# Kernel optimization log

Hardware: AMD Instinct MI355X
Metric: run time of the kernel (lower is better)

The kernel has to match this reference:

```python
import jax, jax.numpy as jnp
import numpy as np

B, S, D, H = 2, 2048, 1024, 16
Dh = D // H
LN_EPS = 1e-5


def setup_inputs() -> dict:
    key = jax.random.key(0)
    ks = jax.random.split(key, 14)
    s = 1.0 / np.sqrt(D)
    return {
        "q": jax.random.normal(ks[0], (B, S, D), jnp.float32),
        "k": jax.random.normal(ks[1], (B, S, D), jnp.float32),
        "v": jax.random.normal(ks[2], (B, S, D), jnp.float32),
        "attn_mask": jax.random.randint(ks[3], (B, S, S), 0, 2).astype(bool),
        "Wq": jax.random.normal(ks[4], (D, D), jnp.float32) * s,
        "bq": jnp.zeros((D,), jnp.float32),
        "Wk": jax.random.normal(ks[5], (D, D), jnp.float32) * s,
        "bk": jnp.zeros((D,), jnp.float32),
        "Wv": jax.random.normal(ks[6], (D, D), jnp.float32) * s,
        "bv": jnp.zeros((D,), jnp.float32),
        "Wo": jax.random.normal(ks[7], (D, D), jnp.float32) * s,
        "bo": jnp.zeros((D,), jnp.float32),
        "gamma": jnp.ones((D,), jnp.float32),
        "beta": jnp.zeros((D,), jnp.float32),
    }


def reference(q, k, v, attn_mask, Wq, bq, Wk, bk, Wv, bv, Wo, bo, gamma, beta):
    residual = q
    # projections (W stored as [in, out])
    qh = (q @ Wq + bq).reshape(B, S, H, Dh).transpose(0, 2, 1, 3)  # [B,H,S,Dh]
    kh = (k @ Wk + bk).reshape(B, S, H, Dh).transpose(0, 2, 1, 3)
    vh = (v @ Wv + bv).reshape(B, S, H, Dh).transpose(0, 2, 1, 3)
    scores = jnp.einsum("bhqd,bhkd->bhqk", qh, kh) / np.sqrt(Dh)
    scores = jnp.where(attn_mask[:, None, :, :], -1e9, scores)
    attn = jax.nn.softmax(scores, axis=-1)  # dropout is identity in eval
    context = jnp.einsum("bhqk,bhkd->bhqd", attn, vh)  # [B,H,S,Dh]
    # faithful to original bug: flat reshape WITHOUT transposing heads back
    context = context.reshape(B, S, D)
    out = context @ Wo + bo
    x = residual + out
    mu = jnp.mean(x, axis=-1, keepdims=True)
    var = jnp.var(x, axis=-1, keepdims=True)
    out = (x - mu) / jnp.sqrt(var + LN_EPS) * gamma + beta
    return out, attn
```

## Files before the change

### kernel.cpp

```cpp
#include <hip/hip_runtime.h>
#include <hip/hip_bf16.h>

typedef __attribute__((ext_vector_type(8))) short bf16x8;
typedef __attribute__((ext_vector_type(4))) float f32x4;

__device__ __forceinline__ short f2bf(float f) {
    union { float f; unsigned u; } v; v.f = f;
    unsigned r = (v.u + 0x7FFFu + ((v.u >> 16) & 1u)) >> 16;
    return (short)r;
}
__device__ __forceinline__ float bf2f(short s) {
    union { unsigned u; float f; } v; v.u = ((unsigned)(unsigned short)s) << 16;
    return v.f;
}
__device__ __forceinline__ void gll16(const void* g, void* l) {
    __builtin_amdgcn_global_load_lds(
        (const __attribute__((address_space(1))) unsigned int*)g,
        (__attribute__((address_space(3))) unsigned int*)l, 16, 0, 0);
}

__global__ __launch_bounds__(256) void k_prep(
    const float* __restrict__ qin, const float* __restrict__ kin, const float* __restrict__ vin,
    short* __restrict__ qbf, short* __restrict__ kbf, short* __restrict__ vbf,
    const float* __restrict__ Wq, const float* __restrict__ Wk,
    const float* __restrict__ Wv, const float* __restrict__ Wo,
    short* __restrict__ WqT, short* __restrict__ WkT,
    short* __restrict__ WvT, short* __restrict__ WoT,
    const int* __restrict__ mask, unsigned* __restrict__ mb)
{
    __shared__ int sm[8192];
    const int bid = blockIdx.x, tid = threadIdx.x;
    if (bid < 6144) {
        const float* in = bid < 2048 ? qin : (bid < 4096 ? kin : vin);
        short* out = bid < 2048 ? qbf : (bid < 4096 ? kbf : vbf);
        const long i = ((long)(bid & 2047) * 256 + tid) * 8;
        float4 f0 = *reinterpret_cast<const float4*>(&in[i]);
        float4 f1 = *reinterpret_cast<const float4*>(&in[i + 4]);
        bf16x8 v;
        v[0] = f2bf(f0.x); v[1] = f2bf(f0.y); v[2] = f2bf(f0.z); v[3] = f2bf(f0.w);
        v[4] = f2bf(f1.x); v[5] = f2bf(f1.y); v[6] = f2bf(f1.z); v[7] = f2bf(f1.w);
        *reinterpret_cast<bf16x8*>(&out[i]) = v;
    } else if (bid < 10240) {
        const int t2 = bid - 6144, which = t2 >> 10, local = t2 & 1023;
        const float* W = which == 0 ? Wq : (which == 1 ? Wk : (which == 2 ? Wv : Wo));
        short* WT = which == 0 ? WqT : (which == 1 ? WkT : (which == 2 ? WvT : WoT));
        float (*t)[33] = reinterpret_cast<float(*)[33]>(sm);
        const int rb = (local >> 5) * 32, cb = (local & 31) * 32;
        const int tr = tid >> 3, tc = (tid & 7) * 4;
        const float4 v = *reinterpret_cast<const float4*>(&W[(long)(rb + tr) * 1024 + cb + tc]);
        t[tr][tc + 0] = v.x; t[tr][tc + 1] = v.y; t[tr][tc + 2] = v.z; t[tr][tc + 3] = v.w;
        __syncthreads();
        short4 o;
        o.x = f2bf(t[tc + 0][tr]); o.y = f2bf(t[tc + 1][tr]);
        o.z = f2bf(t[tc + 2][tr]); o.w = f2bf(t[tc + 3][tr]);
        *reinterpret_cast<short4*>(&WT[(long)(cb + tr) * 1024 + rb + tc]) = o;
    } else {
        const long base = (long)(bid - 10240) * 8192;
#pragma unroll
        for (int i = 0; i < 8; ++i)
            *reinterpret_cast<int4*>(&sm[i * 1024 + tid * 4]) =
                *reinterpret_cast<const int4*>(&mask[base + i * 1024 + tid * 4]);
        __syncthreads();
        unsigned wv = 0;
#pragma unroll
        for (int j = 0; j < 32; ++j) wv |= (sm[tid * 32 + j] != 0 ? 1u : 0u) << j;
        mb[base / 32 + tid] = wv;
    }
}

__global__ __launch_bounds__(256) void k_gemm_qkv(
    const short* __restrict__ A0, const short* __restrict__ A1, const short* __restrict__ A2,
    const short* __restrict__ B0, const short* __restrict__ B1, const short* __restrict__ B2,
    const float* __restrict__ b0, const float* __restrict__ b1, const float* __restrict__ b2,
    short* __restrict__ o0, short* __restrict__ o1, short* __restrict__ o2)
{
    __shared__ short As[128 * 64];
    __shared__ short Bs[128 * 64];
    const int z = blockIdx.z;
    const short* A = z == 0 ? A0 : (z == 1 ? A1 : A2);
    const short* BT = z == 0 ? B0 : (z == 1 ? B1 : B2);
    const float* bias = z == 0 ? b0 : (z == 1 ? b1 : b2);
    short* outp = z == 0 ? o0 : (z == 1 ? o1 : o2);
    const float scale = z == 0 ? 0.125f : 1.0f;

    const int tid = threadIdx.x, w = tid >> 6, lane = tid & 63;
    const int lr = lane & 15, lg = lane >> 4;
    const int rowbase = blockIdx.y * 128, colbase = blockIdx.x * 128;
    const int wr = (w >> 1) * 64, wc = (w & 1) * 64;
    const int srow = lane >> 3, sc_ = (lane & 7) ^ srow;

    f32x4 acc[4][4] = {};

    for (int kb = 0; kb < 1024; kb += 64) {
#pragma unroll
        for (int ii = 0; ii < 4; ++ii) {
            const int rl = w * 32 + ii * 8 + srow;
            gll16(A + (long)(rowbase + rl) * 1024 + kb + sc_ * 8, &As[(w * 32 + ii * 8) * 64]);
            gll16(BT + (long)(colbase + rl) * 1024 + kb + sc_ * 8, &Bs[(w * 32 + ii * 8) * 64]);
        }
        __syncthreads();
#pragma unroll
        for (int ks = 0; ks < 2; ++ks) {
            bf16x8 a[4], bq[4];
#pragma unroll
            for (int m = 0; m < 4; ++m) {
                const int r = wr + m * 16 + lr;
                a[m] = *reinterpret_cast<const bf16x8*>(&As[r * 64 + (((ks * 4 + lg) ^ (r & 7)) << 3)]);
            }
#pragma unroll
            for (int n = 0; n < 4; ++n) {
                const int r = wc + n * 16 + lr;
                bq[n] = *reinterpret_cast<const bf16x8*>(&Bs[r * 64 + (((ks * 4 + lg) ^ (r & 7)) << 3)]);
            }
#pragma unroll
            for (int m = 0; m < 4; ++m)
#pragma unroll
                for (int n = 0; n < 4; ++n)
                    acc[m][n] = __builtin_amdgcn_mfma_f32_16x16x32_bf16(a[m], bq[n], acc[m][n], 0, 0, 0);
        }
        __syncthreads();
    }

#pragma unroll
    for (int m = 0; m < 4; ++m) {
#pragma unroll
        for (int n = 0; n < 4; ++n) {
            const int C = colbase + wc + n * 16 + lr;
            const float bv = bias[C];
#pragma unroll
            for (int rr = 0; rr < 4; ++rr) {
                const int R = rowbase + wr + m * 16 + lg * 4 + rr;
                const float val = (acc[m][n][rr] + bv) * scale;
                const int b = R >> 11, s = R & 2047, h = C >> 6, dh = C & 63;
                if (z != 2)
                    outp[(((long)(b * 16 + h) * 2048 + s) << 6) + dh] = f2bf(val);
                else
                    outp[(((long)(b * 16 + h) * 64 + dh) << 11) + s] = f2bf(val);
            }
        }
    }
}

__global__ __launch_bounds__(256) void k_gemm_o(
    const short* __restrict__ A, const short* __restrict__ BT,
    const float* __restrict__ bias, const float* __restrict__ resid,
    float* __restrict__ outp)
{
    __shared__ short As[128 * 64];
    __shared__ short Bs[128 * 64];
    const int tid = threadIdx.x, w = tid >> 6, lane = tid & 63;
    const int lr = lane & 15, lg = lane >> 4;
    const int rowbase = blockIdx.y * 128, colbase = blockIdx.x * 128;
    const int wr = (w >> 1) * 64, wc = (w & 1) * 64;
    const int srow = lane >> 3, sc_ = (lane & 7) ^ srow;

    f32x4 acc[4][4] = {};

    for (int kb = 0; kb < 1024; kb += 64) {
#pragma unroll
        for (int ii = 0; ii < 4; ++ii) {
            const int rl = w * 32 + ii * 8 + srow;
            gll16(A + (long)(rowbase + rl) * 1024 + kb + sc_ * 8, &As[(w * 32 + ii * 8) * 64]);
            gll16(BT + (long)(colbase + rl) * 1024 + kb + sc_ * 8, &Bs[(w * 32 + ii * 8) * 64]);
        }
        __syncthreads();
#pragma unroll
        for (int ks = 0; ks < 2; ++ks) {
            bf16x8 a[4], bq[4];
#pragma unroll
            for (int m = 0; m < 4; ++m) {
                const int r = wr + m * 16 + lr;
                a[m] = *reinterpret_cast<const bf16x8*>(&As[r * 64 + (((ks * 4 + lg) ^ (r & 7)) << 3)]);
            }
#pragma unroll
            for (int n = 0; n < 4; ++n) {
                const int r = wc + n * 16 + lr;
                bq[n] = *reinterpret_cast<const bf16x8*>(&Bs[r * 64 + (((ks * 4 + lg) ^ (r & 7)) << 3)]);
            }
#pragma unroll
            for (int m = 0; m < 4; ++m)
#pragma unroll
                for (int n = 0; n < 4; ++n)
                    acc[m][n] = __builtin_amdgcn_mfma_f32_16x16x32_bf16(a[m], bq[n], acc[m][n], 0, 0, 0);
        }
        __syncthreads();
    }

#pragma unroll
    for (int m = 0; m < 4; ++m) {
#pragma unroll
        for (int n = 0; n < 4; ++n) {
            const int C = colbase + wc + n * 16 + lr;
            const float bv = bias[C];
#pragma unroll
            for (int rr = 0; rr < 4; ++rr) {
                const int R = rowbase + wr + m * 16 + lg * 4 + rr;
                const long idx = (long)R * 1024 + C;
                outp[idx] = acc[m][n][rr] + bv + resid[idx];
            }
        }
    }
}

__global__ __launch_bounds__(256, 3) void k_attn(
    const short* __restrict__ qh, const short* __restrict__ kh,
    const short* __restrict__ vt, const unsigned* __restrict__ mbits,
    float* __restrict__ attn_out, short* __restrict__ ctxb)
{
    const int g = blockIdx.x, xcd = g & 7, u = g >> 3;
    const int bh = u >> 2, qt = xcd * 4 + (u & 3);
    const int b = bh >> 4;
    const int tid = threadIdx.x, w = tid >> 6, lane = tid & 63;
    const int lr = lane & 15, lg = lane >> 4;
    const int irow = qt * 64 + w * 16;
    const long arow = (long)bh * 2048 + irow;

    __shared__ short Ks[2][64 * 64];
    __shared__ short Vs[2][64 * 64];
    __shared__ short Ps[4][16 * 72];

    const short* qhp = qh + arow * 64;
    const short* khp = kh + (long)bh * 2048 * 64;
    const short* vtp = vt + (long)bh * 64 * 2048;
    const unsigned* mbp = mbits + (long)b * 131072 + (long)irow * 64;

    const bf16x8 aq0 = *reinterpret_cast<const bf16x8*>(&qhp[lr * 64 + lg * 8]);
    const bf16x8 aq1 = *reinterpret_cast<const bf16x8*>(&qhp[lr * 64 + 32 + lg * 8]);

    const int srow = lane >> 3, sc_ = (lane & 7) ^ srow;

    auto stage_k = [&](int buf, int ch) {
#pragma unroll
        for (int ii = 0; ii < 2; ++ii) {
            const int r0 = w * 16 + ii * 8;
            gll16(khp + (long)(ch * 64 + r0 + srow) * 64 + sc_ * 8, &Ks[buf][r0 * 64]);
        }
    };
    auto stage_v = [&](int buf, int ch) {
#pragma unroll
        for (int ii = 0; ii < 2; ++ii) {
            const int r0 = w * 16 + ii * 8;
            gll16(vtp + (long)(r0 + srow) * 2048 + ch * 64 + sc_ * 8, &Vs[buf][r0 * 64]);
        }
    };
    auto kfrag = [&](int buf, int t, int ks) -> bf16x8 {
        const int r = t * 16 + lr;
        return *reinterpret_cast<const bf16x8*>(&Ks[buf][r * 64 + (((ks * 4 + lg) ^ (r & 7)) << 3)]);
    };
    auto vfrag = [&](int buf, int gi, int ks) -> bf16x8 {
        const int r = gi * 16 + lr;
        return *reinterpret_cast<const bf16x8*>(&Vs[buf][r * 64 + (((ks * 4 + lg) ^ (r & 7)) << 3)]);
    };

    float m[4], l[4];
#pragma unroll
    for (int rr = 0; rr < 4; ++rr) { m[rr] = -3.0e38f; l[rr] = 0.f; }
    f32x4 acc[4] = {};

    stage_k(0, 0); stage_v(0, 0);
    asm volatile("s_waitcnt vmcnt(0)" ::: "memory");
    __builtin_amdgcn_s_barrier();
    asm volatile("" ::: "memory");

    for (int ch = 0; ch < 32; ++ch) {
        const int cur = ch & 1;
        unsigned mw[4][2];
#pragma unroll
        for (int rr = 0; rr < 4; ++rr) {
            mw[rr][0] = mbp[(lg * 4 + rr) * 64 + ch * 2];
            mw[rr][1] = mbp[(lg * 4 + rr) * 64 + ch * 2 + 1];
        }
        asm volatile("" ::: "memory");
        if (ch < 31) { stage_k(cur ^ 1, ch + 1); stage_v(cur ^ 1, ch + 1); }
        asm volatile("" ::: "memory");

        f32x4 sct[4];
#pragma unroll
        for (int t = 0; t < 4; ++t) {
            f32x4 sc = {};
            sc = __builtin_amdgcn_mfma_f32_16x16x32_bf16(aq0, kfrag(cur, t, 0), sc, 0, 0, 0);
            sc = __builtin_amdgcn_mfma_f32_16x16x32_bf16(aq1, kfrag(cur, t, 1), sc, 0, 0, 0);
#pragma unroll
            for (int rr = 0; rr < 4; ++rr) {
                const bool masked = (mw[rr][t >> 1] >> (((t & 1) << 4) + lr)) & 1;
                sct[t][rr] = masked ? -1e9f : sc[rr];
            }
        }
        float f[4];
#pragma unroll
        for (int rr = 0; rr < 4; ++rr) {
            float c = fmaxf(fmaxf(sct[0][rr], sct[1][rr]), fmaxf(sct[2][rr], sct[3][rr]));
#pragma unroll
            for (int off = 1; off < 16; off <<= 1) c = fmaxf(c, __shfl_xor(c, off, 16));
            const bool bump = c > m[rr] + 8.0f;
            const float mn = bump ? c : m[rr];
            f[rr] = bump ? __expf(m[rr] - mn) : 1.0f;
            m[rr] = mn;
        }
        float esum[4] = {0.f, 0.f, 0.f, 0.f};
#pragma unroll
        for (int t = 0; t < 4; ++t)
#pragma unroll
            for (int rr = 0; rr < 4; ++rr) {
                const float p = __expf(sct[t][rr] - m[rr]);
                esum[rr] += p;
                Ps[w][(lg * 4 + rr) * 72 + t * 16 + lr] = f2bf(p);
            }
#pragma unroll
        for (int rr = 0; rr < 4; ++rr) l[rr] = l[rr] * f[rr] + esum[rr];
#pragma unroll
        for (int gi = 0; gi < 4; ++gi)
#pragma unroll
            for (int rr = 0; rr < 4; ++rr) acc[gi][rr] *= f[rr];

        const bf16x8 pa0 = *reinterpret_cast<const bf16x8*>(&Ps[w][lr * 72 + lg * 8]);
        const bf16x8 pa1 = *reinterpret_cast<const bf16x8*>(&Ps[w][lr * 72 + 32 + lg * 8]);
#pragma unroll
        for (int gi = 0; gi < 4; ++gi) {
            acc[gi] = __builtin_amdgcn_mfma_f32_16x16x32_bf16(pa0, vfrag(cur, gi, 0), acc[gi], 0, 0, 0);
            acc[gi] = __builtin_amdgcn_mfma_f32_16x16x32_bf16(pa1, vfrag(cur, gi, 1), acc[gi], 0, 0, 0);
        }
        asm volatile("s_waitcnt vmcnt(0)" ::: "memory");
        __builtin_amdgcn_s_barrier();
        asm volatile("" ::: "memory");
    }

    float mf[4], il[4];
#pragma unroll
    for (int rr = 0; rr < 4; ++rr) {
        float lw = l[rr];
#pragma unroll
        for (int off = 1; off < 16; off <<= 1) lw += __shfl_xor(lw, off, 16);
        il[rr] = 1.0f / lw;
        mf[rr] = m[rr];
    }
#pragma unroll
    for (int gi = 0; gi < 4; ++gi)
#pragma unroll
        for (int rr = 0; rr < 4; ++rr)
            ctxb[(arow + lg * 4 + rr) * 64 + gi * 16 + lr] = f2bf(acc[gi][rr] * il[rr]);

    stage_k(0, 0);
    asm volatile("s_waitcnt vmcnt(0)" ::: "memory");
    __builtin_amdgcn_s_barrier();
    asm volatile("" ::: "memory");

    for (int ch = 0; ch < 32; ++ch) {
        const int cur = ch & 1;
        unsigned mw[4][2];
#pragma unroll
        for (int rr = 0; rr < 4; ++rr) {
            mw[rr][0] = mbp[(lg * 4 + rr) * 64 + ch * 2];
            mw[rr][1] = mbp[(lg * 4 + rr) * 64 + ch * 2 + 1];
        }
        asm volatile("" ::: "memory");
        if (ch < 31) stage_k(cur ^ 1, ch + 1);
        asm volatile("" ::: "memory");

#pragma unroll
        for (int t = 0; t < 4; ++t) {
            f32x4 sc = {};
            sc = __builtin_amdgcn_mfma_f32_16x16x32_bf16(aq0, kfrag(cur, t, 0), sc, 0, 0, 0);
            sc = __builtin_amdgcn_mfma_f32_16x16x32_bf16(aq1, kfrag(cur, t, 1), sc, 0, 0, 0);
#pragma unroll
            for (int rr = 0; rr < 4; ++rr) {
                const bool masked = (mw[rr][t >> 1] >> (((t & 1) << 4) + lr)) & 1;
                const float s = masked ? -1e9f : sc[rr];
                const float p = __expf(s - mf[rr]) * il[rr];
                Ps[w][(lg * 4 + rr) * 72 + t * 16 + lr] = f2bf(p);
            }
        }
#pragma unroll
        for (int i2 = 0; i2 < 4; ++i2) {
            const int r = i2 * 4 + lg;
            const short4 p4 = *reinterpret_cast<const short4*>(&Ps[w][r * 72 + lr * 4]);
            float4 o;
            o.x = bf2f(p4.x); o.y = bf2f(p4.y); o.z = bf2f(p4.z); o.w = bf2f(p4.w);
            *reinterpret_cast<float4*>(&attn_out[(arow + r) * 2048 + ch * 64 + lr * 4]) = o;
        }
        asm volatile("s_waitcnt vmcnt(4)" ::: "memory");
        __builtin_amdgcn_s_barrier();
        asm volatile("" ::: "memory");
    }
}

__global__ __launch_bounds__(256) void k_ln(const float* __restrict__ x,
    const float* __restrict__ gamma, const float* __restrict__ beta,
    float* __restrict__ out)
{
    __shared__ float red[8];
    const int r = blockIdx.x, tid = threadIdx.x;
    const float4 v = reinterpret_cast<const float4*>(x + (long)r * 1024)[tid];
    float s = v.x + v.y + v.z + v.w;
    float q2 = v.x * v.x + v.y * v.y + v.z * v.z + v.w * v.w;
#pragma unroll
    for (int off = 32; off; off >>= 1) {
        s += __shfl_xor(s, off, 64);
        q2 += __shfl_xor(q2, off, 64);
    }
    if ((tid & 63) == 0) { red[(tid >> 6) * 2] = s; red[(tid >> 6) * 2 + 1] = q2; }
    __syncthreads();
    s = red[0] + red[2] + red[4] + red[6];
    q2 = red[1] + red[3] + red[5] + red[7];
    const float mu = s * (1.0f / 1024.0f);
    const float var = q2 * (1.0f / 1024.0f) - mu * mu;
    const float rs = rsqrtf(var + 1e-5f);
    const float4 gm = reinterpret_cast<const float4*>(gamma)[tid];
    const float4 bb = reinterpret_cast<const float4*>(beta)[tid];
    float4 o;
    o.x = (v.x - mu) * rs * gm.x + bb.x;
    o.y = (v.y - mu) * rs * gm.y + bb.y;
    o.z = (v.z - mu) * rs * gm.z + bb.z;
    o.w = (v.w - mu) * rs * gm.w + bb.w;
    reinterpret_cast<float4*>(out + (long)r * 1024)[tid] = o;
}

extern "C" void kernel_launch(void* const* d_in, const int* in_sizes, int n_in,
                              void* d_out, int out_size, void* d_ws, size_t ws_size,
                              hipStream_t stream)
{
    const float* qin  = (const float*)d_in[0];
    const float* kin  = (const float*)d_in[1];
    const float* vin  = (const float*)d_in[2];
    const int*   mask = (const int*)d_in[3];
    const float* Wq = (const float*)d_in[4];
    const float* bq = (const float*)d_in[5];
    const float* Wk = (const float*)d_in[6];
    const float* bk = (const float*)d_in[7];
    const float* Wv = (const float*)d_in[8];
    const float* bv = (const float*)d_in[9];
    const float* Wo = (const float*)d_in[10];
    const float* bo = (const float*)d_in[11];
    const float* gamma = (const float*)d_in[12];
    const float* beta  = (const float*)d_in[13];

    char* ws = (char*)d_ws;
    short* WqT = (short*)(ws + (0ul  << 20));
    short* WkT = (short*)(ws + (2ul  << 20));
    short* WvT = (short*)(ws + (4ul  << 20));
    short* WoT = (short*)(ws + (6ul  << 20));
    short* qbf = (short*)(ws + (8ul  << 20));
    short* kbf = (short*)(ws + (16ul << 20));
    short* vbf = (short*)(ws + (24ul << 20));
    short* qh  = (short*)(ws + (32ul << 20));
    short* khb = (short*)(ws + (40ul << 20));
    short* vtb = (short*)(ws + (48ul << 20));
    unsigned* mb = (unsigned*)(ws + (56ul << 20));
    short* ctxb = (short*)(ws + (57ul << 20));
    float* xb   = (float*)(ws + (8ul  << 20));

    float* outLN = (float*)d_out;
    float* attnO = (float*)d_out + 4194304;

    const dim3 blk(256);
    k_prep<<<dim3(11264), blk, 0, stream>>>(qin, kin, vin, qbf, kbf, vbf,
                                            Wq, Wk, Wv, Wo, WqT, WkT, WvT, WoT, mask, mb);
    k_gemm_qkv<<<dim3(8, 32, 3), blk, 0, stream>>>(qbf, kbf, vbf, WqT, WkT, WvT,
                                                   bq, bk, bv, qh, khb, vtb);
    k_attn<<<dim3(1024), blk, 0, stream>>>(qh, khb, vtb, mb, attnO, ctxb);
    k_gemm_o<<<dim3(8, 32), blk, 0, stream>>>(ctxb, WoT, bo, qin, xb);
    k_ln<<<dim3(4096), blk, 0, stream>>>(xb, gamma, beta, outLN);
}
```

Before: 362.2 us.

## Drop LDS staging in attention; load K/V fragments directly from global memory

Removes the double-buffered LDS staging of K and V tiles, along with the block barriers. Each wave now loads its MFMA operand fragments directly from global memory and relies on L2 for reuse across waves. The block-to-(bh, q-tile) mapping is changed so that blocks sharing a head land on the same XCD. The second pass now writes attention probabilities straight to global memory as uncoalesced fp32 scalars instead of going through a bf16 LDS round trip, which also raises output precision. The risk is more global traffic and latency, and poorly coalesced attention stores.

```diff
diff --git a/kernel.cpp b/kernel.cpp
--- a/kernel.cpp
+++ b/kernel.cpp
@@ -207,79 +207,46 @@
     const short* __restrict__ vt, const unsigned* __restrict__ mbits,
     float* __restrict__ attn_out, short* __restrict__ ctxb)
 {
-    const int g = blockIdx.x, xcd = g & 7, u = g >> 3;
-    const int bh = u >> 2, qt = xcd * 4 + (u & 3);
+    const int g = blockIdx.x;
+    const int bh = (g & 7) * 4 + ((g >> 3) & 3);
+    const int qt = g >> 5;
     const int b = bh >> 4;
     const int tid = threadIdx.x, w = tid >> 6, lane = tid & 63;
     const int lr = lane & 15, lg = lane >> 4;
     const int irow = qt * 64 + w * 16;
     const long arow = (long)bh * 2048 + irow;
 
-    __shared__ short Ks[2][64 * 64];
-    __shared__ short Vs[2][64 * 64];
     __shared__ short Ps[4][16 * 72];
 
     const short* qhp = qh + arow * 64;
-    const short* khp = kh + (long)bh * 2048 * 64;
-    const short* vtp = vt + (long)bh * 64 * 2048;
+    const short* khp = kh + (long)bh * 131072;
+    const short* vtp = vt + (long)bh * 131072;
     const unsigned* mbp = mbits + (long)b * 131072 + (long)irow * 64;
 
     const bf16x8 aq0 = *reinterpret_cast<const bf16x8*>(&qhp[lr * 64 + lg * 8]);
     const bf16x8 aq1 = *reinterpret_cast<const bf16x8*>(&qhp[lr * 64 + 32 + lg * 8]);
 
-    const int srow = lane >> 3, sc_ = (lane & 7) ^ srow;
-
-    auto stage_k = [&](int buf, int ch) {
-#pragma unroll
-        for (int ii = 0; ii < 2; ++ii) {
-            const int r0 = w * 16 + ii * 8;
-            gll16(khp + (long)(ch * 64 + r0 + srow) * 64 + sc_ * 8, &Ks[buf][r0 * 64]);
-        }
-    };
-    auto stage_v = [&](int buf, int ch) {
-#pragma unroll
-        for (int ii = 0; ii < 2; ++ii) {
-            const int r0 = w * 16 + ii * 8;
-            gll16(vtp + (long)(r0 + srow) * 2048 + ch * 64 + sc_ * 8, &Vs[buf][r0 * 64]);
-        }
-    };
-    auto kfrag = [&](int buf, int t, int ks) -> bf16x8 {
-        const int r = t * 16 + lr;
-        return *reinterpret_cast<const bf16x8*>(&Ks[buf][r * 64 + (((ks * 4 + lg) ^ (r & 7)) << 3)]);
-    };
-    auto vfrag = [&](int buf, int gi, int ks) -> bf16x8 {
-        const int r = gi * 16 + lr;
-        return *reinterpret_cast<const bf16x8*>(&Vs[buf][r * 64 + (((ks * 4 + lg) ^ (r & 7)) << 3)]);
-    };
-
     float m[4], l[4];
 #pragma unroll
     for (int rr = 0; rr < 4; ++rr) { m[rr] = -3.0e38f; l[rr] = 0.f; }
     f32x4 acc[4] = {};
 
-    stage_k(0, 0); stage_v(0, 0);
-    asm volatile("s_waitcnt vmcnt(0)" ::: "memory");
-    __builtin_amdgcn_s_barrier();
-    asm volatile("" ::: "memory");
-
     for (int ch = 0; ch < 32; ++ch) {
-        const int cur = ch & 1;
         unsigned mw[4][2];
 #pragma unroll
         for (int rr = 0; rr < 4; ++rr) {
             mw[rr][0] = mbp[(lg * 4 + rr) * 64 + ch * 2];
             mw[rr][1] = mbp[(lg * 4 + rr) * 64 + ch * 2 + 1];
         }
-        asm volatile("" ::: "memory");
-        if (ch < 31) { stage_k(cur ^ 1, ch + 1); stage_v(cur ^ 1, ch + 1); }
-        asm volatile("" ::: "memory");
-
+        const short* kc = khp + (long)ch * 64 * 64;
         f32x4 sct[4];
 #pragma unroll
         for (int t = 0; t < 4; ++t) {
+            const bf16x8 k0 = *reinterpret_cast<const bf16x8*>(&kc[(t * 16 + lr) * 64 + lg * 8]);
+            const bf16x8 k1 = *reinterpret_cast<const bf16x8*>(&kc[(t * 16 + lr) * 64 + 32 + lg * 8]);
             f32x4 sc = {};
-            sc = __builtin_amdgcn_mfma_f32_16x16x32_bf16(aq0, kfrag(cur, t, 0), sc, 0, 0, 0);
-            sc = __builtin_amdgcn_mfma_f32_16x16x32_bf16(aq1, kfrag(cur, t, 1), sc, 0, 0, 0);
+            sc = __builtin_amdgcn_mfma_f32_16x16x32_bf16(aq0, k0, sc, 0, 0, 0);
+            sc = __builtin_amdgcn_mfma_f32_16x16x32_bf16(aq1, k1, sc, 0, 0, 0);
 #pragma unroll
             for (int rr = 0; rr < 4; ++rr) {
                 const bool masked = (mw[rr][t >> 1] >> (((t & 1) << 4) + lr)) & 1;
@@ -315,24 +282,23 @@
 
         const bf16x8 pa0 = *reinterpret_cast<const bf16x8*>(&Ps[w][lr * 72 + lg * 8]);
         const bf16x8 pa1 = *reinterpret_cast<const bf16x8*>(&Ps[w][lr * 72 + 32 + lg * 8]);
+        const short* vc = vtp + ch * 64;
 #pragma unroll
         for (int gi = 0; gi < 4; ++gi) {
-            acc[gi] = __builtin_amdgcn_mfma_f32_16x16x32_bf16(pa0, vfrag(cur, gi, 0), acc[gi], 0, 0, 0);
-            acc[gi] = __builtin_amdgcn_mfma_f32_16x16x32_bf16(pa1, vfrag(cur, gi, 1), acc[gi], 0, 0, 0);
-        }
-        asm volatile("s_waitcnt vmcnt(0)" ::: "memory");
-        __builtin_amdgcn_s_barrier();
-        asm volatile("" ::: "memory");
-    }
-
-    float mf[4], il[4];
+            const bf16x8 v0 = *reinterpret_cast<const bf16x8*>(&vc[(long)(gi * 16 + lr) * 2048 + lg * 8]);
+            const bf16x8 v1 = *reinterpret_cast<const bf16x8*>(&vc[(long)(gi * 16 + lr) * 2048 + 32 + lg * 8]);
+            acc[gi] = __builtin_amdgcn_mfma_f32_16x16x32_bf16(pa0, v0, acc[gi], 0, 0, 0);
+            acc[gi] = __builtin_amdgcn_mfma_f32_16x16x32_bf16(pa1, v1, acc[gi], 0, 0, 0);
+        }
+    }
+
+    float il[4];
 #pragma unroll
     for (int rr = 0; rr < 4; ++rr) {
         float lw = l[rr];
 #pragma unroll
         for (int off = 1; off < 16; off <<= 1) lw += __shfl_xor(lw, off, 16);
         il[rr] = 1.0f / lw;
-        mf[rr] = m[rr];
     }
 #pragma unroll
     for (int gi = 0; gi < 4; ++gi)
@@ -340,47 +306,29 @@
         for (int rr = 0; rr < 4; ++rr)
             ctxb[(arow + lg * 4 + rr) * 64 + gi * 16 + lr] = f2bf(acc[gi][rr] * il[rr]);
 
-    stage_k(0, 0);
-    asm volatile("s_waitcnt vmcnt(0)" ::: "memory");
-    __builtin_amdgcn_s_barrier();
-    asm volatile("" ::: "memory");
-
     for (int ch = 0; ch < 32; ++ch) {
-        const int cur = ch & 1;
         unsigned mw[4][2];
 #pragma unroll
         for (int rr = 0; rr < 4; ++rr) {
             mw[rr][0] = mbp[(lg * 4 + rr) * 64 + ch * 2];
             mw[rr][1] = mbp[(lg * 4 + rr) * 64 + ch * 2 + 1];
         }
-        asm volatile("" ::: "memory");
-        if (ch < 31) stage_k(cur ^ 1, ch + 1);
-        asm volatile("" ::: "memory");
-
+        const short* kc = khp + (long)ch * 64 * 64;
 #pragma unroll
         for (int t = 0; t < 4; ++t) {
+            const bf16x8 k0 = *reinterpret_cast<const bf16x8*>(&kc[(t * 16 + lr) * 64 + lg * 8]);
+            const bf16x8 k1 = *reinterpret_cast<const bf16x8*>(&kc[(t * 16 + lr) * 64 + 32 + lg * 8]);
             f32x4 sc = {};
-            sc = __builtin_amdgcn_mfma_f32_16x16x32_bf16(aq0, kfrag(cur, t, 0), sc, 0, 0, 0);
-            sc = __builtin_amdgcn_mfma_f32_16x16x32_bf16(aq1, kfrag(cur, t, 1), sc, 0, 0, 0);
+            sc = __builtin_amdgcn_mfma_f32_16x16x32_bf16(aq0, k0, sc, 0, 0, 0);
+            sc = __builtin_amdgcn_mfma_f32_16x16x32_bf16(aq1, k1, sc, 0, 0, 0);
 #pragma unroll
             for (int rr = 0; rr < 4; ++rr) {
                 const bool masked = (mw[rr][t >> 1] >> (((t & 1) << 4) + lr)) & 1;
                 const float s = masked ? -1e9f : sc[rr];
-                const float p = __expf(s - mf[rr]) * il[rr];
-                Ps[w][(lg * 4 + rr) * 72 + t * 16 + lr] = f2bf(p);
-            }
-        }
-#pragma unroll
-        for (int i2 = 0; i2 < 4; ++i2) {
-            const int r = i2 * 4 + lg;
-            const short4 p4 = *reinterpret_cast<const short4*>(&Ps[w][r * 72 + lr * 4]);
-            float4 o;
-            o.x = bf2f(p4.x); o.y = bf2f(p4.y); o.z = bf2f(p4.z); o.w = bf2f(p4.w);
-            *reinterpret_cast<float4*>(&attn_out[(arow + r) * 2048 + ch * 64 + lr * 4]) = o;
-        }
-        asm volatile("s_waitcnt vmcnt(4)" ::: "memory");
-        __builtin_amdgcn_s_barrier();
-        asm volatile("" ::: "memory");
+                const float p = __expf(s - m[rr]) * il[rr];
+                attn_out[(arow + lg * 4 + rr) * 2048 + ch * 64 + t * 16 + lr] = p;
+            }
+        }
     }
 }
 
```

Measured after the change: 567.1 us. 1.57x slower.

## Split attention into score kernel with partial softmax stats and output kernel

Applied to the files above, without the earlier changes.

Adds a two-pass attention path. A tiled QK^T kernel writes masked bf16 scores plus per-tile row max and exp-sum, and a second kernel merges those statistics, recomputes the probabilities, writes the fp32 attention matrix and accumulates P·V. The path is chosen only when the workspace is large enough to hold the 256 MB bf16 score buffer, otherwise the fused kernel still runs. It trades extra HBM traffic for writing and re-reading scores against better parallelism and no recomputation, and the scores are rounded to bf16 before softmax.

```diff
diff --git a/kernel.cpp b/kernel.cpp
--- a/kernel.cpp
+++ b/kernel.cpp
@@ -18,6 +18,8 @@
         (const __attribute__((address_space(1))) unsigned int*)g,
         (__attribute__((address_space(3))) unsigned int*)l, 16, 0, 0);
 }
+
+#define MASKF (-998244352.0f)
 
 __global__ __launch_bounds__(256) void k_prep(
     const float* __restrict__ qin, const float* __restrict__ kin, const float* __restrict__ vin,
@@ -202,6 +204,174 @@
     }
 }
 
+__global__ __launch_bounds__(256) void k_score(
+    const short* __restrict__ qh, const short* __restrict__ kh,
+    const unsigned* __restrict__ mbits, short* __restrict__ S,
+    float* __restrict__ pmax, float* __restrict__ plsum)
+{
+    __shared__ short As[128 * 64];
+    __shared__ short Bs[128 * 64];
+    __shared__ float sm_[4][64];
+    __shared__ float sl_[4][64];
+    const int bh = blockIdx.z, b = bh >> 4;
+    const int rowbase = blockIdx.y * 128, colbase = blockIdx.x * 128;
+    const int tid = threadIdx.x, w = tid >> 6, lane = tid & 63;
+    const int lr = lane & 15, lg = lane >> 4;
+    const int wr = (w >> 1) * 64, wc = (w & 1) * 64;
+    const int srow = lane >> 3, sc_ = (lane & 7) ^ srow;
+    const short* A = qh + (long)bh * 131072;
+    const short* BT = kh + (long)bh * 131072;
+    const unsigned* mbp = mbits + (long)b * 131072;
+
+#pragma unroll
+    for (int ii = 0; ii < 4; ++ii) {
+        const int rl = w * 32 + ii * 8 + srow;
+        gll16(A + (long)(rowbase + rl) * 64 + sc_ * 8, &As[(w * 32 + ii * 8) * 64]);
+        gll16(BT + (long)(colbase + rl) * 64 + sc_ * 8, &Bs[(w * 32 + ii * 8) * 64]);
+    }
+    __syncthreads();
+
+    f32x4 acc[4][4] = {};
+#pragma unroll
+    for (int ks = 0; ks < 2; ++ks) {
+        bf16x8 a[4], bq[4];
+#pragma unroll
+        for (int m = 0; m < 4; ++m) {
+            const int r = wr + m * 16 + lr;
+            a[m] = *reinterpret_cast<const bf16x8*>(&As[r * 64 + (((ks * 4 + lg) ^ (r & 7)) << 3)]);
+        }
+#pragma unroll
+        for (int n = 0; n < 4; ++n) {
+            const int r = wc + n * 16 + lr;
+            bq[n] = *reinterpret_cast<const bf16x8*>(&Bs[r * 64 + (((ks * 4 + lg) ^ (r & 7)) << 3)]);
+        }
+#pragma unroll
+        for (int m = 0; m < 4; ++m)
+#pragma unroll
+            for (int n = 0; n < 4; ++n)
+                acc[m][n] = __builtin_amdgcn_mfma_f32_16x16x32_bf16(a[m], bq[n], acc[m][n], 0, 0, 0);
+    }
+
+#pragma unroll
+    for (int m = 0; m < 4; ++m) {
+#pragma unroll
+        for (int rr = 0; rr < 4; ++rr) {
+            const int R = rowbase + wr + m * 16 + lg * 4 + rr;
+            const unsigned mw0 = mbp[R * 64 + ((colbase + wc) >> 5)];
+            const unsigned mw1 = mbp[R * 64 + ((colbase + wc) >> 5) + 1];
+            float sv[4];
+#pragma unroll
+            for (int n = 0; n < 4; ++n) {
+                const bool masked = (((n < 2) ? mw0 : mw1) >> (((n & 1) << 4) + lr)) & 1;
+                sv[n] = masked ? MASKF : acc[m][n][rr];
+                S[((long)bh * 2048 + R) * 2048 + colbase + wc + n * 16 + lr] = f2bf(sv[n]);
+            }
+            float mx = fmaxf(fmaxf(sv[0], sv[1]), fmaxf(sv[2], sv[3]));
+#pragma unroll
+            for (int off = 1; off < 16; off <<= 1) mx = fmaxf(mx, __shfl_xor(mx, off, 16));
+            float es = __expf(sv[0] - mx) + __expf(sv[1] - mx) +
+                       __expf(sv[2] - mx) + __expf(sv[3] - mx);
+#pragma unroll
+            for (int off = 1; off < 16; off <<= 1) es += __shfl_xor(es, off, 16);
+            if (lr == 0) {
+                sm_[w][m * 16 + lg * 4 + rr] = mx;
+                sl_[w][m * 16 + lg * 4 + rr] = es;
+            }
+        }
+    }
+    __syncthreads();
+    if (tid < 128) {
+        const int R = tid, wlo = (R >> 6) * 2, ri = R & 63;
+        const float m1 = sm_[wlo][ri], m2 = sm_[wlo + 1][ri];
+        const float mm = fmaxf(m1, m2);
+        const float ll = sl_[wlo][ri] * __expf(m1 - mm) + sl_[wlo + 1][ri] * __expf(m2 - mm);
+        const long sidx = ((long)bh * 2048 + rowbase + R) * 16 + blockIdx.x;
+        pmax[sidx] = mm;
+        plsum[sidx] = ll;
+    }
+}
+
+__global__ __launch_bounds__(256) void k_attnout(
+    const short* __restrict__ S, const float* __restrict__ pmax,
+    const float* __restrict__ plsum, const short* __restrict__ vt,
+    float* __restrict__ attn_out, short* __restrict__ ctxb)
+{
+    const int g = blockIdx.x;
+    const int bh = (g & 7) * 4 + ((g >> 3) & 3);
+    const int qt = g >> 5;
+    const int tid = threadIdx.x, w = tid >> 6, lane = tid & 63;
+    const int lr = lane & 15, lg = lane >> 4;
+    const int irow = qt * 64 + w * 16;
+    const long arow = (long)bh * 2048 + irow;
+    __shared__ short Ps[4][16 * 72];
+
+    float m_, il_;
+    {
+        const float4* pm4 = reinterpret_cast<const float4*>(pmax + (arow + lr) * 16);
+        const float4* pl4 = reinterpret_cast<const float4*>(plsum + (arow + lr) * 16);
+        const float4 a0 = pm4[0], a1 = pm4[1], a2 = pm4[2], a3 = pm4[3];
+        m_ = fmaxf(fmaxf(fmaxf(a0.x, a0.y), fmaxf(a0.z, a0.w)),
+                   fmaxf(fmaxf(fmaxf(a1.x, a1.y), fmaxf(a1.z, a1.w)),
+                         fmaxf(fmaxf(fmaxf(a2.x, a2.y), fmaxf(a2.z, a2.w)),
+                               fmaxf(fmaxf(a3.x, a3.y), fmaxf(a3.z, a3.w)))));
+        const float4 b0 = pl4[0], b1 = pl4[1], b2 = pl4[2], b3 = pl4[3];
+        float l = b0.x * __expf(a0.x - m_) + b0.y * __expf(a0.y - m_) +
+                  b0.z * __expf(a0.z - m_) + b0.w * __expf(a0.w - m_) +
+                  b1.x * __expf(a1.x - m_) + b1.y * __expf(a1.y - m_) +
+                  b1.z * __expf(a1.z - m_) + b1.w * __expf(a1.w - m_) +
+                  b2.x * __expf(a2.x - m_) + b2.y * __expf(a2.y - m_) +
+                  b2.z * __expf(a2.z - m_) + b2.w * __expf(a2.w - m_) +
+                  b3.x * __expf(a3.x - m_) + b3.y * __expf(a3.y - m_) +
+                  b3.z * __expf(a3.z - m_) + b3.w * __expf(a3.w - m_);
+        il_ = 1.0f / l;
+    }
+    const int rowA = lane >> 3, colA = (lane & 7) * 8;
+    const float mA = __shfl(m_, rowA, 16),     iA = __shfl(il_, rowA, 16);
+    const float mB = __shfl(m_, rowA + 8, 16), iB = __shfl(il_, rowA + 8, 16);
+
+    const short* Sp = S + arow * 2048;
+    const short* vtp = vt + (long)bh * 131072;
+    f32x4 acc[4] = {};
+
+    for (int ch = 0; ch < 32; ++ch) {
+        const bf16x8 sa = *reinterpret_cast<const bf16x8*>(&Sp[(long)rowA * 2048 + ch * 64 + colA]);
+        const bf16x8 sb = *reinterpret_cast<const bf16x8*>(&Sp[(long)(rowA + 8) * 2048 + ch * 64 + colA]);
+        float pa[8], pb[8];
+#pragma unroll
+        for (int j = 0; j < 8; ++j) {
+            pa[j] = __expf(bf2f(sa[j]) - mA) * iA;
+            pb[j] = __expf(bf2f(sb[j]) - mB) * iB;
+        }
+        float* oa = &attn_out[(arow + rowA) * 2048 + ch * 64 + colA];
+        float* ob = &attn_out[(arow + rowA + 8) * 2048 + ch * 64 + colA];
+        *reinterpret_cast<float4*>(oa)     = make_float4(pa[0], pa[1], pa[2], pa[3]);
+        *reinterpret_cast<float4*>(oa + 4) = make_float4(pa[4], pa[5], pa[6], pa[7]);
+        *reinterpret_cast<float4*>(ob)     = make_float4(pb[0], pb[1], pb[2], pb[3]);
+        *reinterpret_cast<float4*>(ob + 4) = make_float4(pb[4], pb[5], pb[6], pb[7]);
+
+        bf16x8 ea, eb;
+#pragma unroll
+        for (int j = 0; j < 8; ++j) { ea[j] = f2bf(pa[j]); eb[j] = f2bf(pb[j]); }
+        *reinterpret_cast<bf16x8*>(&Ps[w][rowA * 72 + colA]) = ea;
+        *reinterpret_cast<bf16x8*>(&Ps[w][(rowA + 8) * 72 + colA]) = eb;
+
+        const bf16x8 pa0 = *reinterpret_cast<const bf16x8*>(&Ps[w][lr * 72 + lg * 8]);
+        const bf16x8 pa1 = *reinterpret_cast<const bf16x8*>(&Ps[w][lr * 72 + 32 + lg * 8]);
+#pragma unroll
+        for (int gi = 0; gi < 4; ++gi) {
+            const bf16x8 v0 = *reinterpret_cast<const bf16x8*>(&vtp[(long)(gi * 16 + lr) * 2048 + ch * 64 + lg * 8]);
+            const bf16x8 v1 = *reinterpret_cast<const bf16x8*>(&vtp[(long)(gi * 16 + lr) * 2048 + ch * 64 + 32 + lg * 8]);
+            acc[gi] = __builtin_amdgcn_mfma_f32_16x16x32_bf16(pa0, v0, acc[gi], 0, 0, 0);
+            acc[gi] = __builtin_amdgcn_mfma_f32_16x16x32_bf16(pa1, v1, acc[gi], 0, 0, 0);
+        }
+    }
+#pragma unroll
+    for (int gi = 0; gi < 4; ++gi)
+#pragma unroll
+        for (int rr = 0; rr < 4; ++rr)
+            ctxb[(arow + lg * 4 + rr) * 64 + gi * 16 + lr] = f2bf(acc[gi][rr]);
+}
+
 __global__ __launch_bounds__(256, 3) void k_attn(
     const short* __restrict__ qh, const short* __restrict__ kh,
     const short* __restrict__ vt, const unsigned* __restrict__ mbits,
@@ -220,13 +390,12 @@
     __shared__ short Ps[4][16 * 72];
 
     const short* qhp = qh + arow * 64;
-    const short* khp = kh + (long)bh * 2048 * 64;
-    const short* vtp = vt + (long)bh * 64 * 2048;
+    const short* khp = kh + (long)bh * 131072;
+    const short* vtp = vt + (long)bh * 131072;
     const unsigned* mbp = mbits + (long)b * 131072 + (long)irow * 64;
 
     const bf16x8 aq0 = *reinterpret_cast<const bf16x8*>(&qhp[lr * 64 + lg * 8]);
     const bf16x8 aq1 = *reinterpret_cast<const bf16x8*>(&qhp[lr * 64 + 32 + lg * 8]);
-
     const int srow = lane >> 3, sc_ = (lane & 7) ^ srow;
 
     auto stage_k = [&](int buf, int ch) {
@@ -439,25 +608,35 @@
     short* WkT = (short*)(ws + (2ul  << 20));
     short* WvT = (short*)(ws + (4ul  << 20));
     short* WoT = (short*)(ws + (6ul  << 20));
-    short* qbf = (short*)(ws + (8ul  << 20));
-    short* kbf = (short*)(ws + (16ul << 20));
-    short* vbf = (short*)(ws + (24ul << 20));
-    short* qh  = (short*)(ws + (32ul << 20));
-    short* khb = (short*)(ws + (40ul << 20));
-    short* vtb = (short*)(ws + (48ul << 20));
-    unsigned* mb = (unsigned*)(ws + (56ul << 20));
-    short* ctxb = (short*)(ws + (57ul << 20));
-    float* xb   = (float*)(ws + (8ul  << 20));
+    short* qh  = (short*)(ws + (8ul  << 20));
+    short* khb = (short*)(ws + (16ul << 20));
+    short* vtb = (short*)(ws + (24ul << 20));
+    unsigned* mb = (unsigned*)(ws + (32ul << 20));
+    short* ctxb = (short*)(ws + (33ul << 20));
+    float* pmax  = (float*)(ws + (41ul << 20));
+    float* plsum = (float*)(ws + (45ul << 20));
+    short* qbf = (short*)(ws + (49ul << 20));
+    short* kbf = (short*)(ws + (57ul << 20));
+    short* vbf = (short*)(ws + (65ul << 20));
+    short* Sb  = (short*)(ws + (49ul << 20));
+    float* xb  = (float*)(ws + (49ul << 20));
 
     float* outLN = (float*)d_out;
     float* attnO = (float*)d_out + 4194304;
+
+    const bool big = ws_size >= (305ul << 20);
 
     const dim3 blk(256);
     k_prep<<<dim3(11264), blk, 0, stream>>>(qin, kin, vin, qbf, kbf, vbf,
                                             Wq, Wk, Wv, Wo, WqT, WkT, WvT, WoT, mask, mb);
     k_gemm_qkv<<<dim3(8, 32, 3), blk, 0, stream>>>(qbf, kbf, vbf, WqT, WkT, WvT,
                                                    bq, bk, bv, qh, khb, vtb);
-    k_attn<<<dim3(1024), blk, 0, stream>>>(qh, khb, vtb, mb, attnO, ctxb);
+    if (big) {
+        k_score<<<dim3(16, 16, 32), blk, 0, stream>>>(qh, khb, mb, Sb, pmax, plsum);
+        k_attnout<<<dim3(1024), blk, 0, stream>>>(Sb, pmax, plsum, vtb, attnO, ctxb);
+    } else {
+        k_attn<<<dim3(1024), blk, 0, stream>>>(qh, khb, vtb, mb, attnO, ctxb);
+    }
     k_gemm_o<<<dim3(8, 32), blk, 0, stream>>>(ctxb, WoT, bo, qin, xb);
     k_ln<<<dim3(4096), blk, 0, stream>>>(xb, gamma, beta, outLN);
 }
```

Measured after the change: 572.5 us. 1.58x slower.

## Restructure attention into stats-only first pass and fused PV second pass

Applied to the files above, without the earlier changes.

The first attention pass now computes only per-row max and sum statistics, using an online lane-local update in base 2, with the log2(e) factor folded into the Q projection scale. This removes the P@V MFMAs, the LDS P writes and the V loads from that pass. The second pass writes the exact normalized probabilities and also does the P@V accumulation, so context is produced already normalized. K staging becomes triple-buffered with relaxed waitcnt values so loads run further ahead. The cost is more LDS, more registers for the per-tile stats, and V loads plus MFMAs added to the second pass, which may lower occupancy.

```diff
diff --git a/kernel.cpp b/kernel.cpp
--- a/kernel.cpp
+++ b/kernel.cpp
@@ -18,6 +18,8 @@
         (const __attribute__((address_space(1))) unsigned int*)g,
         (__attribute__((address_space(3))) unsigned int*)l, 16, 0, 0);
 }
+
+#define QSCALE 0.18033688011112042f
 
 __global__ __launch_bounds__(256) void k_prep(
     const float* __restrict__ qin, const float* __restrict__ kin, const float* __restrict__ vin,
@@ -81,7 +83,7 @@
     const short* BT = z == 0 ? B0 : (z == 1 ? B1 : B2);
     const float* bias = z == 0 ? b0 : (z == 1 ? b1 : b2);
     short* outp = z == 0 ? o0 : (z == 1 ? o1 : o2);
-    const float scale = z == 0 ? 0.125f : 1.0f;
+    const float scale = z == 0 ? QSCALE : 1.0f;
 
     const int tid = threadIdx.x, w = tid >> 6, lane = tid & 63;
     const int lr = lane & 15, lg = lane >> 4;
@@ -215,18 +217,17 @@
     const int irow = qt * 64 + w * 16;
     const long arow = (long)bh * 2048 + irow;
 
-    __shared__ short Ks[2][64 * 64];
+    __shared__ short Ks[3][64 * 64];
     __shared__ short Vs[2][64 * 64];
     __shared__ short Ps[4][16 * 72];
 
     const short* qhp = qh + arow * 64;
-    const short* khp = kh + (long)bh * 2048 * 64;
-    const short* vtp = vt + (long)bh * 64 * 2048;
+    const short* khp = kh + (long)bh * 131072;
+    const short* vtp = vt + (long)bh * 131072;
     const unsigned* mbp = mbits + (long)b * 131072 + (long)irow * 64;
 
     const bf16x8 aq0 = *reinterpret_cast<const bf16x8*>(&qhp[lr * 64 + lg * 8]);
     const bf16x8 aq1 = *reinterpret_cast<const bf16x8*>(&qhp[lr * 64 + 32 + lg * 8]);
-
     const int srow = lane >> 3, sc_ = (lane & 7) ^ srow;
 
     auto stage_k = [&](int buf, int ch) {
@@ -252,29 +253,26 @@
         return *reinterpret_cast<const bf16x8*>(&Vs[buf][r * 64 + (((ks * 4 + lg) ^ (r & 7)) << 3)]);
     };
 
-    float m[4], l[4];
-#pragma unroll
-    for (int rr = 0; rr < 4; ++rr) { m[rr] = -3.0e38f; l[rr] = 0.f; }
-    f32x4 acc[4] = {};
-
-    stage_k(0, 0); stage_v(0, 0);
+    float m[4][4], l[4][4];
+#pragma unroll
+    for (int t = 0; t < 4; ++t)
+#pragma unroll
+        for (int rr = 0; rr < 4; ++rr) { m[t][rr] = -3.0e38f; l[t][rr] = 0.f; }
+
+    stage_k(0, 0); stage_k(1, 1);
     asm volatile("s_waitcnt vmcnt(0)" ::: "memory");
     __builtin_amdgcn_s_barrier();
     asm volatile("" ::: "memory");
 
     for (int ch = 0; ch < 32; ++ch) {
-        const int cur = ch & 1;
+        const int cur = ch % 3;
         unsigned mw[4][2];
 #pragma unroll
         for (int rr = 0; rr < 4; ++rr) {
             mw[rr][0] = mbp[(lg * 4 + rr) * 64 + ch * 2];
             mw[rr][1] = mbp[(lg * 4 + rr) * 64 + ch * 2 + 1];
         }
-        asm volatile("" ::: "memory");
-        if (ch < 31) { stage_k(cur ^ 1, ch + 1); stage_v(cur ^ 1, ch + 1); }
-        asm volatile("" ::: "memory");
-
-        f32x4 sct[4];
+        stage_k((ch + 2) % 3, (ch + 2) & 31);
 #pragma unroll
         for (int t = 0; t < 4; ++t) {
             f32x4 sc = {};
@@ -283,79 +281,52 @@
 #pragma unroll
             for (int rr = 0; rr < 4; ++rr) {
                 const bool masked = (mw[rr][t >> 1] >> (((t & 1) << 4) + lr)) & 1;
-                sct[t][rr] = masked ? -1e9f : sc[rr];
-            }
-        }
-        float f[4];
-#pragma unroll
-        for (int rr = 0; rr < 4; ++rr) {
-            float c = fmaxf(fmaxf(sct[0][rr], sct[1][rr]), fmaxf(sct[2][rr], sct[3][rr]));
-#pragma unroll
-            for (int off = 1; off < 16; off <<= 1) c = fmaxf(c, __shfl_xor(c, off, 16));
-            const bool bump = c > m[rr] + 8.0f;
-            const float mn = bump ? c : m[rr];
-            f[rr] = bump ? __expf(m[rr] - mn) : 1.0f;
-            m[rr] = mn;
-        }
-        float esum[4] = {0.f, 0.f, 0.f, 0.f};
-#pragma unroll
-        for (int t = 0; t < 4; ++t)
-#pragma unroll
-            for (int rr = 0; rr < 4; ++rr) {
-                const float p = __expf(sct[t][rr] - m[rr]);
-                esum[rr] += p;
-                Ps[w][(lg * 4 + rr) * 72 + t * 16 + lr] = f2bf(p);
-            }
-#pragma unroll
-        for (int rr = 0; rr < 4; ++rr) l[rr] = l[rr] * f[rr] + esum[rr];
-#pragma unroll
-        for (int gi = 0; gi < 4; ++gi)
-#pragma unroll
-            for (int rr = 0; rr < 4; ++rr) acc[gi][rr] *= f[rr];
-
-        const bf16x8 pa0 = *reinterpret_cast<const bf16x8*>(&Ps[w][lr * 72 + lg * 8]);
-        const bf16x8 pa1 = *reinterpret_cast<const bf16x8*>(&Ps[w][lr * 72 + 32 + lg * 8]);
-#pragma unroll
-        for (int gi = 0; gi < 4; ++gi) {
-            acc[gi] = __builtin_amdgcn_mfma_f32_16x16x32_bf16(pa0, vfrag(cur, gi, 0), acc[gi], 0, 0, 0);
-            acc[gi] = __builtin_amdgcn_mfma_f32_16x16x32_bf16(pa1, vfrag(cur, gi, 1), acc[gi], 0, 0, 0);
-        }
-        asm volatile("s_waitcnt vmcnt(0)" ::: "memory");
+                const float s = masked ? -1e9f : sc[rr];
+                const float d = s - m[t][rr];
+                const float e = exp2f(-fabsf(d));
+                const bool gt = d > 0.f;
+                l[t][rr] = gt ? l[t][rr] * e + 1.f : l[t][rr] + e;
+                m[t][rr] = gt ? s : m[t][rr];
+            }
+        }
+        asm volatile("s_waitcnt vmcnt(2)" ::: "memory");
         __builtin_amdgcn_s_barrier();
         asm volatile("" ::: "memory");
     }
 
-    float mf[4], il[4];
+    float C[4];
 #pragma unroll
     for (int rr = 0; rr < 4; ++rr) {
-        float lw = l[rr];
-#pragma unroll
-        for (int off = 1; off < 16; off <<= 1) lw += __shfl_xor(lw, off, 16);
-        il[rr] = 1.0f / lw;
-        mf[rr] = m[rr];
-    }
-#pragma unroll
-    for (int gi = 0; gi < 4; ++gi)
-#pragma unroll
-        for (int rr = 0; rr < 4; ++rr)
-            ctxb[(arow + lg * 4 + rr) * 64 + gi * 16 + lr] = f2bf(acc[gi][rr] * il[rr]);
-
-    stage_k(0, 0);
+        float M = fmaxf(fmaxf(m[0][rr], m[1][rr]), fmaxf(m[2][rr], m[3][rr]));
+        float L = l[0][rr] * exp2f(m[0][rr] - M) + l[1][rr] * exp2f(m[1][rr] - M) +
+                  l[2][rr] * exp2f(m[2][rr] - M) + l[3][rr] * exp2f(m[3][rr] - M);
+#pragma unroll
+        for (int off = 1; off < 16; off <<= 1) {
+            const float Mo = __shfl_xor(M, off, 16);
+            const float Lo = __shfl_xor(L, off, 16);
+            const float Mn = fmaxf(M, Mo);
+            L = L * exp2f(M - Mn) + Lo * exp2f(Mo - Mn);
+            M = Mn;
+        }
+        C[rr] = M + log2f(L);
+    }
+
+    f32x4 acc[4] = {};
+    stage_v(0, 0); stage_k(0, 0); stage_k(1, 1);
     asm volatile("s_waitcnt vmcnt(0)" ::: "memory");
     __builtin_amdgcn_s_barrier();
     asm volatile("" ::: "memory");
 
     for (int ch = 0; ch < 32; ++ch) {
-        const int cur = ch & 1;
+        const int cur = ch % 3;
         unsigned mw[4][2];
 #pragma unroll
         for (int rr = 0; rr < 4; ++rr) {
             mw[rr][0] = mbp[(lg * 4 + rr) * 64 + ch * 2];
             mw[rr][1] = mbp[(lg * 4 + rr) * 64 + ch * 2 + 1];
         }
-        asm volatile("" ::: "memory");
-        if (ch < 31) stage_k(cur ^ 1, ch + 1);
-        asm volatile("" ::: "memory");
+        stage_v((ch + 1) & 1, (ch + 1) & 31);
+        stage_k((ch + 2) % 3, (ch + 2) & 31);
 
 #pragma unroll
         for (int t = 0; t < 4; ++t) {
@@ -366,7 +337,7 @@
             for (int rr = 0; rr < 4; ++rr) {
                 const bool masked = (mw[rr][t >> 1] >> (((t & 1) << 4) + lr)) & 1;
                 const float s = masked ? -1e9f : sc[rr];
-                const float p = __expf(s - mf[rr]) * il[rr];
+                const float p = exp2f(s - C[rr]);
                 Ps[w][(lg * 4 + rr) * 72 + t * 16 + lr] = f2bf(p);
             }
         }
@@ -378,10 +349,23 @@
             o.x = bf2f(p4.x); o.y = bf2f(p4.y); o.z = bf2f(p4.z); o.w = bf2f(p4.w);
             *reinterpret_cast<float4*>(&attn_out[(arow + r) * 2048 + ch * 64 + lr * 4]) = o;
         }
-        asm volatile("s_waitcnt vmcnt(4)" ::: "memory");
+        const bf16x8 pa0 = *reinterpret_cast<const bf16x8*>(&Ps[w][lr * 72 + lg * 8]);
+        const bf16x8 pa1 = *reinterpret_cast<const bf16x8*>(&Ps[w][lr * 72 + 32 + lg * 8]);
+#pragma unroll
+        for (int gi = 0; gi < 4; ++gi) {
+            acc[gi] = __builtin_amdgcn_mfma_f32_16x16x32_bf16(pa0, vfrag(ch & 1, gi, 0), acc[gi], 0, 0, 0);
+            acc[gi] = __builtin_amdgcn_mfma_f32_16x16x32_bf16(pa1, vfrag(ch & 1, gi, 1), acc[gi], 0, 0, 0);
+        }
+        asm volatile("s_waitcnt vmcnt(6)" ::: "memory");
         __builtin_amdgcn_s_barrier();
         asm volatile("" ::: "memory");
     }
+
+#pragma unroll
+    for (int gi = 0; gi < 4; ++gi)
+#pragma unroll
+        for (int rr = 0; rr < 4; ++rr)
+            ctxb[(arow + lg * 4 + rr) * 64 + gi * 16 + lr] = f2bf(acc[gi][rr]);
 }
 
 __global__ __launch_bounds__(256) void k_ln(const float* __restrict__ x,
```

Result: slower. 384.9 us (+6.3%).
